# Optimization experiments

Hardware: AMD Instinct MI355X
Metric: run time of the kernel (lower is better)

## Reference

```python
import jax, jax.numpy as jnp
import numpy as np

B, S, D = 8, 4096, 256
L, H = 4, 8
HD = D // H  # head_dim = 32
EPS = 1e-5


def layer_norm(x, gamma, beta):
    mu = jnp.mean(x, axis=-1, keepdims=True)
    var = jnp.mean(jnp.square(x - mu), axis=-1, keepdims=True)
    return (x - mu) * jax.lax.rsqrt(var + EPS) * gamma + beta


def setup_inputs() -> dict:
    key = jax.random.key(0)
    ks = jax.random.split(key, 9)
    sc = 0.02
    x = jax.random.normal(ks[0], (B, S, D), dtype=jnp.float32)
    # per-head projection weights, torch Linear convention: (out=head_dim, in=D)
    Wq = jax.random.normal(ks[1], (L, H, HD, D), dtype=jnp.float32) * sc
    Wk = jax.random.normal(ks[2], (L, H, HD, D), dtype=jnp.float32) * sc
    Wv = jax.random.normal(ks[3], (L, H, HD, D), dtype=jnp.float32) * sc
    W1 = jax.random.normal(ks[4], (L, D, D), dtype=jnp.float32) * sc
    b1 = jax.random.normal(ks[5], (L, D), dtype=jnp.float32) * sc
    W2 = jax.random.normal(ks[6], (L, D, D), dtype=jnp.float32) * sc
    b2 = jax.random.normal(ks[7], (L, D), dtype=jnp.float32) * sc
    gamma = jnp.ones((D,), dtype=jnp.float32)
    beta = jnp.zeros((D,), dtype=jnp.float32)
    return {"processed_grid_repr": x, "Wq": Wq, "Wk": Wk, "Wv": Wv,
            "W1": W1, "b1": b1, "W2": W2, "b2": b2,
            "gamma": gamma, "beta": beta}


def reference(processed_grid_repr, Wq, Wk, Wv, W1, b1, W2, b2, gamma, beta):
    out = processed_grid_repr  # (B, S, D)
    scale = 1.0 / jnp.sqrt(jnp.float32(S))  # original scales by sqrt(seq_len)
    for l in range(L):
        h = layer_norm(out, gamma, beta)
        # all heads at once: (B, H, S, HD)
        Q = jnp.einsum('bsd,hed->bhse', h, Wq[l])
        K = jnp.einsum('bsd,hed->bhse', h, Wk[l])
        V = jnp.einsum('bsd,hed->bhse', h, Wv[l])
        # original does key.reshape(B, HD, S) (a RESHAPE, not a transpose)
        Kr = K.reshape(B, H, HD, S)
        # original einsum 'bqq,bqd->bqd' only uses the diagonal of QK^r,
        # so compute only the diagonal: diag[b,h,q] = sum_e Q[b,h,q,e]*Kr[b,h,e,q]
        diag = jnp.einsum('bhse,bhes->bhs', Q, Kr) * scale
        attn = diag[..., None] * V  # (B, H, S, HD)
        # concat heads along last dim (head order preserved)
        msa_out = attn.transpose(0, 2, 1, 3).reshape(B, S, D)
        attended = msa_out + out
        m = layer_norm(attended, gamma, beta)
        m = jax.nn.gelu(m @ W1[l].T + b1[l], approximate=False)
        m = jax.nn.gelu(m @ W2[l].T + b2[l], approximate=False)
        out = m + attended
    # final: layer norm of CLS-like token 0
    return layer_norm(out[:, 0, :], gamma, beta)  # (B, D)
```

## Files before the change

kernel.cpp:

```cpp
#include <hip/hip_runtime.h>
#include <hip/hip_bf16.h>
#include <hip/hip_fp16.h>

typedef _Float16 half_t;
typedef _Float16 half8 __attribute__((ext_vector_type(8)));
typedef _Float16 half4 __attribute__((ext_vector_type(4)));
typedef float f32x4 __attribute__((ext_vector_type(4)));

#define BB 8
#define SS 4096
#define DD 256
#define HH 8
#define LL 4
#define MTOT (BB*SS)

__device__ inline float gelu_f(float v) { return 0.5f * v * (1.0f + erff(v * 0.70710678118f)); }
__device__ inline half8 splat8(half_t v) { return (half8){v, v, v, v, v, v, v, v}; }

__device__ __forceinline__ void gload16(const half_t* g, half_t* l) {
    __builtin_amdgcn_global_load_lds(
        (const __attribute__((address_space(1))) void*)g,
        (__attribute__((address_space(3))) void*)l, 16, 0, 0);
}

__global__ __launch_bounds__(256) void prep_weights(
    const float* __restrict__ Wq, const float* __restrict__ Wk, const float* __restrict__ Wv,
    const float* __restrict__ W1, const float* __restrict__ b1,
    const float* __restrict__ W2, const float* __restrict__ b2,
    const float* __restrict__ gamma, const float* __restrict__ beta,
    half_t* __restrict__ Wall, half_t* __restrict__ W1h, half_t* __restrict__ W2h,
    float* __restrict__ bqkv, float* __restrict__ b1f, float* __restrict__ b2f)
{
    int blk = blockIdx.x;
    int l = blk / 5, type = blk % 5;
    int o = threadIdx.x;
    const float* src = (type == 0 ? Wq : type == 1 ? Wk : type == 2 ? Wv : type == 3 ? W1 : W2)
                       + ((size_t)l * 256 + o) * 256;
    half_t* dsth = (type < 3) ? Wall + ((size_t)(l * 3 + type) * 256 + o) * 256
                 : (type == 3) ? W1h + ((size_t)l * 256 + o) * 256
                               : W2h + ((size_t)l * 256 + o) * 256;
    float acc = 0.f;
    for (int d4 = 0; d4 < 64; ++d4) {
        float4 w = *(const float4*)(src + d4 * 4);
        half4 hv;
        if (type == 4) {
            hv = half4{ (half_t)w.x, (half_t)w.y, (half_t)w.z, (half_t)w.w };
        } else {
            float4 g = *(const float4*)(gamma + d4 * 4);
            float4 bt = *(const float4*)(beta + d4 * 4);
            acc += w.x * bt.x + w.y * bt.y + w.z * bt.z + w.w * bt.w;
            hv = half4{ (half_t)(w.x * g.x), (half_t)(w.y * g.y), (half_t)(w.z * g.z), (half_t)(w.w * g.w) };
        }
        *(half4*)(dsth + d4 * 4) = hv;
    }
    if (type < 3) bqkv[(l * 3 + type) * 256 + o] = acc;
    else if (type == 3) b1f[l * 256 + o] = b1[l * 256 + o] + acc;
    else b2f[l * 256 + o] = b2[l * 256 + o];
}

__global__ __launch_bounds__(256) void cvt_x(const float* __restrict__ in, half_t* __restrict__ out) {
    int i = (blockIdx.x * 256 + threadIdx.x) * 4;
    float4 v = *(const float4*)(in + i);
    half4 h = { (half_t)v.x, (half_t)v.y, (half_t)v.z, (half_t)v.w };
    *(half4*)(out + i) = h;
}

__global__ __launch_bounds__(256) void row_stats(const half_t* __restrict__ in,
                                                 float2* __restrict__ st) {
    int wave = threadIdx.x >> 6, lane = threadIdx.x & 63;
    int row = blockIdx.x * 4 + wave;
    size_t base = (size_t)row * DD + lane * 4;
    half4 x4 = *(const half4*)(in + base);
    float a0 = x4[0], a1 = x4[1], a2 = x4[2], a3 = x4[3];
    float s1 = a0 + a1 + a2 + a3;
    float s2 = a0 * a0 + a1 * a1 + a2 * a2 + a3 * a3;
    #pragma unroll
    for (int m = 32; m; m >>= 1) {
        s1 += __shfl_xor(s1, m);
        s2 += __shfl_xor(s2, m);
    }
    if (lane == 0) {
        float mu = s1 * (1.0f / DD);
        float var = s2 * (1.0f / DD) - mu * mu;
        st[row] = make_float2(mu, rsqrtf(var + 1e-5f));
    }
}

__device__ inline void xcd_remap(int& bx, int& by, int& bz) {
    int lin = blockIdx.x + gridDim.x * (blockIdx.y + gridDim.y * blockIdx.z);
    int nyz = gridDim.y * gridDim.z;
    int xcd = lin & 7;
    int slot = lin >> 3;
    int yz = slot % nyz;
    int xi = slot / nyz;
    bx = xcd + 8 * xi;
    by = yz % gridDim.y;
    bz = yz / gridDim.y;
}

template<int NORM, int EPI>
__global__ __launch_bounds__(256) void gemm128(const half_t* __restrict__ A,
                                               const float2* __restrict__ statsA,
                                               const half_t* __restrict__ Wbase,
                                               const float* __restrict__ biasBase,
                                               const half_t* __restrict__ resid,
                                               half_t* __restrict__ o0,
                                               half_t* __restrict__ o1,
                                               half_t* __restrict__ o2) {
    const int t = threadIdx.x, lane = t & 63, wavei = t >> 6;
    const int wm = wavei >> 1, wn = wavei & 1, r = lane & 15, g = lane >> 4;
    int bx, by, bz;
    xcd_remap(bx, by, bz);
    const int row0 = bx * 128, col0 = by * 128;
    const half_t* W = Wbase + (size_t)bz * 65536;
    const float* bias = biasBase + bz * 256;
    half_t* outp = (bz == 0) ? o0 : ((bz == 1) ? o1 : o2);

    __shared__ __align__(16) half_t lds[2][16384];

    const half_t* Ag = A + (size_t)row0 * DD;
    const half_t* Wg = W + (size_t)col0 * DD;

    half8 sA[4], bA[4];
    if (NORM) {
        #pragma unroll
        for (int mt = 0; mt < 4; ++mt) {
            float2 st = statsA[row0 + wm * 64 + mt * 16 + r];
            sA[mt] = splat8((half_t)st.y);
            bA[mt] = splat8((half_t)(-st.x * st.y));
        }
    }

    int rowS[4], chS[4];
    #pragma unroll
    for (int i = 0; i < 4; ++i) {
        int G = i * 256 + t;
        rowS[i] = G >> 3;
        chS[i] = ((G & 7) ^ (rowS[i] & 7)) * 8;
    }

    #pragma unroll
    for (int i = 0; i < 4; ++i) {
        int G = i * 256 + t;
        gload16(Ag + (size_t)rowS[i] * DD + chS[i], &lds[0][G * 8]);
        gload16(Wg + (size_t)rowS[i] * DD + chS[i], &lds[0][8192 + G * 8]);
    }
    __syncthreads();

    f32x4 acc[4][4];
    #pragma unroll
    for (int i = 0; i < 4; ++i)
        #pragma unroll
        for (int j = 0; j < 4; ++j) acc[i][j] = (f32x4){0.f, 0.f, 0.f, 0.f};

    #pragma unroll
    for (int stp = 0; stp < 4; ++stp) {
        const int cur = stp & 1;
        if (stp < 3) {
            int kk = (stp + 1) * 64;
            #pragma unroll
            for (int i = 0; i < 4; ++i) {
                int G = i * 256 + t;
                gload16(Ag + (size_t)rowS[i] * DD + kk + chS[i], &lds[cur ^ 1][G * 8]);
                gload16(Wg + (size_t)rowS[i] * DD + kk + chS[i], &lds[cur ^ 1][8192 + G * 8]);
            }
        }
        #pragma unroll
        for (int ks = 0; ks < 2; ++ks) {
            half8 af[4], bf[4];
            #pragma unroll
            for (int mt = 0; mt < 4; ++mt) {
                int rw = wm * 64 + mt * 16 + r;
                int cc = (ks * 4 + g) ^ (rw & 7);
                half8 raw = *(const half8*)&lds[cur][rw * 64 + cc * 8];
                af[mt] = NORM ? (half8)(raw * sA[mt] + bA[mt]) : raw;
            }
            #pragma unroll
            for (int nt = 0; nt < 4; ++nt) {
                int rw = wn * 64 + nt * 16 + r;
                int cc = (ks * 4 + g) ^ (rw & 7);
                bf[nt] = *(const half8*)&lds[cur][8192 + rw * 64 + cc * 8];
            }
            #pragma unroll
            for (int mt = 0; mt < 4; ++mt)
                #pragma unroll
                for (int nt = 0; nt < 4; ++nt)
                    acc[mt][nt] = __builtin_amdgcn_mfma_f32_16x16x32_f16(af[mt], bf[nt], acc[mt][nt], 0, 0, 0);
        }
        __syncthreads();
    }

    half_t* ldsT = &lds[0][0];
    #pragma unroll
    for (int mt = 0; mt < 4; ++mt) {
        #pragma unroll
        for (int nt = 0; nt < 4; ++nt) {
            int colL = wn * 64 + nt * 16 + r;
            float bv = bias[col0 + colL];
            #pragma unroll
            for (int j = 0; j < 4; ++j) {
                int rowL = wm * 64 + mt * 16 + g * 4 + j;
                float v = acc[mt][nt][j] + bv;
                if (EPI != 0) v = gelu_f(v);
                ldsT[rowL * 128 + (colL ^ ((rowL & 12) << 2))] = (half_t)v;
            }
        }
    }
    __syncthreads();
    const int l15 = lane & 15, lg = lane >> 4;
    #pragma unroll
    for (int i = 0; i < 8; ++i) {
        int rowL = wavei * 32 + lg * 8 + i;
        int colL = l15 * 8;
        half8 v = *(const half8*)&ldsT[rowL * 128 + (colL ^ ((rowL & 12) << 2))];
        size_t off = (size_t)(row0 + rowL) * DD + col0 + colL;
        if (EPI == 2) {
            half8 rsd = *(const half8*)&resid[off];
            #pragma unroll
            for (int q = 0; q < 8; ++q) v[q] = (half_t)((float)v[q] + (float)rsd[q]);
        }
        *(half8*)&outp[off] = v;
    }
}

__global__ __launch_bounds__(256) void diag_tiled(const half_t* __restrict__ Q,
                                                  const half_t* __restrict__ K,
                                                  float* __restrict__ dg) {
    int blk = blockIdx.x;
    int sblk = blk & 15, h = (blk >> 4) & 7, b = blk >> 7;
    int t = threadIdx.x;
    __shared__ __align__(16) half_t kt[256 * 32];
    int r0b = sblk * 8;
    {
        int e = t >> 3, del = t & 7;
        const half_t* kp = K + ((size_t)b * SS + e * 128 + r0b + del) * DD + h * 32;
        int4* dst = (int4*)&kt[t * 32];
        const int4* sp = (const int4*)kp;
        dst[0] = sp[0]; dst[1] = sp[1]; dst[2] = sp[2]; dst[3] = sp[3];
    }
    __syncthreads();
    int s = sblk * 256 + t;
    const half8* q8 = (const half8*)(Q + ((size_t)b * SS + s) * DD + h * 32);
    int cs = t & 31, ds = t >> 5;
    float sum = 0.f;
    #pragma unroll
    for (int v = 0; v < 4; ++v) {
        half8 qq = q8[v];
        #pragma unroll
        for (int j = 0; j < 8; ++j) {
            int e = v * 8 + j;
            sum += (float)qq[j] * (float)kt[(e * 8 + ds) * 32 + cs];
        }
    }
    dg[((size_t)b << 15) | ((size_t)h << 12) | s] = sum * 0.015625f;
}

__global__ __launch_bounds__(256) void attn_stat(const half_t* __restrict__ resid,
                                                 const half_t* __restrict__ V,
                                                 const float* __restrict__ dg,
                                                 half_t* __restrict__ att,
                                                 float2* __restrict__ st2) {
    int wave = threadIdx.x >> 6, lane = threadIdx.x & 63;
    int row = blockIdx.x * 4 + wave;
    int b = row >> 12, s = row & (SS - 1);
    int h = lane >> 3;
    float dgv = dg[((size_t)b << 15) | ((size_t)h << 12) | s];
    size_t base = (size_t)row * DD + lane * 4;
    half4 rs4 = *(const half4*)(resid + base);
    half4 v4 = *(const half4*)(V + base);
    float a0 = (float)rs4[0] + dgv * (float)v4[0];
    float a1 = (float)rs4[1] + dgv * (float)v4[1];
    float a2 = (float)rs4[2] + dgv * (float)v4[2];
    float a3 = (float)rs4[3] + dgv * (float)v4[3];
    half4 at = { (half_t)a0, (half_t)a1, (half_t)a2, (half_t)a3 };
    *(half4*)(att + base) = at;
    float s1 = a0 + a1 + a2 + a3;
    float s2 = a0 * a0 + a1 * a1 + a2 * a2 + a3 * a3;
    #pragma unroll
    for (int m = 32; m; m >>= 1) {
        s1 += __shfl_xor(s1, m);
        s2 += __shfl_xor(s2, m);
    }
    if (lane == 0) {
        float mu = s1 * (1.0f / DD);
        float var = s2 * (1.0f / DD) - mu * mu;
        st2[row] = make_float2(mu, rsqrtf(var + 1e-5f));
    }
}

__global__ __launch_bounds__(256) void final_ln_kernel(const half_t* __restrict__ cur,
                                                       float* __restrict__ out,
                                                       const float* __restrict__ gamma,
                                                       const float* __restrict__ beta) {
    int b = blockIdx.x;
    int d = threadIdx.x;
    float x = (float)cur[(size_t)b * SS * DD + d];
    float s1 = x, s2 = x * x;
    #pragma unroll
    for (int m = 32; m; m >>= 1) {
        s1 += __shfl_xor(s1, m);
        s2 += __shfl_xor(s2, m);
    }
    __shared__ float ls1[4], ls2[4];
    int wave = threadIdx.x >> 6, lane = threadIdx.x & 63;
    if (lane == 0) { ls1[wave] = s1; ls2[wave] = s2; }
    __syncthreads();
    float t1 = ls1[0] + ls1[1] + ls1[2] + ls1[3];
    float t2 = ls2[0] + ls2[1] + ls2[2] + ls2[3];
    float mu = t1 * (1.0f / DD);
    float var = t2 * (1.0f / DD) - mu * mu;
    float rs = rsqrtf(var + 1e-5f);
    out[(size_t)b * DD + d] = (x - mu) * rs * gamma[d] + beta[d];
}

extern "C" void kernel_launch(void* const* d_in, const int* in_sizes, int n_in,
                              void* d_out, int out_size, void* d_ws, size_t ws_size,
                              hipStream_t stream) {
    const float* x     = (const float*)d_in[0];
    const float* Wq    = (const float*)d_in[1];
    const float* Wk    = (const float*)d_in[2];
    const float* Wv    = (const float*)d_in[3];
    const float* W1    = (const float*)d_in[4];
    const float* b1    = (const float*)d_in[5];
    const float* W2    = (const float*)d_in[6];
    const float* b2    = (const float*)d_in[7];
    const float* gamma = (const float*)d_in[8];
    const float* beta  = (const float*)d_in[9];

    char* p = (char*)d_ws;
    half_t* x16  = (half_t*)p; p += (size_t)MTOT * DD * 2;
    half_t* cur  = (half_t*)p; p += (size_t)MTOT * DD * 2;
    half_t* att  = (half_t*)p; p += (size_t)MTOT * DD * 2;
    half_t* Qb   = (half_t*)p; p += (size_t)MTOT * DD * 2;
    half_t* Kb   = (half_t*)p; p += (size_t)MTOT * DD * 2;
    half_t* Vb   = (half_t*)p; p += (size_t)MTOT * DD * 2;
    half_t* m1   = (half_t*)p; p += (size_t)MTOT * DD * 2;
    float*  dgp  = (float*)p;  p += (size_t)BB * HH * SS * 4;
    float2* stA  = (float2*)p; p += (size_t)MTOT * 8;
    float2* stB  = (float2*)p; p += (size_t)MTOT * 8;
    half_t* Wall = (half_t*)p; p += (size_t)LL * 3 * 65536 * 2;
    half_t* W1h  = (half_t*)p; p += (size_t)LL * 65536 * 2;
    half_t* W2h  = (half_t*)p; p += (size_t)LL * 65536 * 2;
    float*  bqkv = (float*)p;  p += (size_t)LL * 3 * 256 * 4;
    float*  b1f  = (float*)p;  p += (size_t)LL * 256 * 4;
    float*  b2f  = (float*)p;  p += (size_t)LL * 256 * 4;

    prep_weights<<<LL * 5, 256, 0, stream>>>(Wq, Wk, Wv, W1, b1, W2, b2, gamma, beta,
                                             Wall, W1h, W2h, bqkv, b1f, b2f);
    cvt_x<<<8192, 256, 0, stream>>>(x, x16);

    const half_t* curin = x16;
    for (int l = 0; l < LL; ++l) {
        row_stats<<<MTOT / 4, 256, 0, stream>>>(curin, stA);
        gemm128<1, 0><<<dim3(256, 2, 3), 256, 0, stream>>>(
            curin, stA, Wall + (size_t)l * 3 * 65536, bqkv + l * 3 * 256, nullptr, Qb, Kb, Vb);
        diag_tiled<<<1024, 256, 0, stream>>>(Qb, Kb, dgp);
        attn_stat<<<MTOT / 4, 256, 0, stream>>>(curin, Vb, dgp, att, stB);
        gemm128<1, 1><<<dim3(256, 2, 1), 256, 0, stream>>>(
            att, stB, W1h + (size_t)l * 65536, b1f + l * 256, nullptr, m1, m1, m1);
        gemm128<0, 2><<<dim3(256, 2, 1), 256, 0, stream>>>(
            m1, nullptr, W2h + (size_t)l * 65536, b2f + l * 256, att, cur, cur, cur);
        curin = cur;
    }
    final_ln_kernel<<<BB, 256, 0, stream>>>(cur, (float*)d_out, gamma, beta);
}
```

Before: 369.7 us.

## Fuse FFN GEMMs into one kernel keeping intermediate in LDS, fold row stats

Replaces the two separate FFN GEMM launches with one kernel. Each block takes 64 rows, applies the layer-norm affine on the fly, computes GELU(W1) into shared memory, then runs the W2 GEMM, residual add and GELU from shared memory. It writes the new activations and their row statistics for the next layer's LN, which removes the separate row_stats launch. The input conversion is also merged with the first row-stats pass. This avoids the m1 round trip through global memory and several launches, at the cost of about 80KB of LDS per block (lower occupancy) and a 64-row tile with 512 blocks.

After: 362.3 us. -2.0%, faster.

```diff
diff --git a/kernel.cpp b/kernel.cpp
--- a/kernel.cpp
+++ b/kernel.cpp
@@ -58,22 +58,17 @@
     else b2f[l * 256 + o] = b2[l * 256 + o];
 }
 
-__global__ __launch_bounds__(256) void cvt_x(const float* __restrict__ in, half_t* __restrict__ out) {
-    int i = (blockIdx.x * 256 + threadIdx.x) * 4;
-    float4 v = *(const float4*)(in + i);
-    half4 h = { (half_t)v.x, (half_t)v.y, (half_t)v.z, (half_t)v.w };
-    *(half4*)(out + i) = h;
-}
-
-__global__ __launch_bounds__(256) void row_stats(const half_t* __restrict__ in,
-                                                 float2* __restrict__ st) {
+__global__ __launch_bounds__(256) void cvt_x_stats(const float* __restrict__ in,
+                                                   half_t* __restrict__ out,
+                                                   float2* __restrict__ st) {
     int wave = threadIdx.x >> 6, lane = threadIdx.x & 63;
     int row = blockIdx.x * 4 + wave;
-    size_t base = (size_t)row * DD + lane * 4;
-    half4 x4 = *(const half4*)(in + base);
-    float a0 = x4[0], a1 = x4[1], a2 = x4[2], a3 = x4[3];
-    float s1 = a0 + a1 + a2 + a3;
-    float s2 = a0 * a0 + a1 * a1 + a2 * a2 + a3 * a3;
+    const float* ip = in + (size_t)row * DD + lane * 4;
+    float4 v = *(const float4*)ip;
+    half4 h = { (half_t)v.x, (half_t)v.y, (half_t)v.z, (half_t)v.w };
+    *(half4*)(out + (size_t)row * DD + lane * 4) = h;
+    float s1 = v.x + v.y + v.z + v.w;
+    float s2 = v.x * v.x + v.y * v.y + v.z * v.z + v.w * v.w;
     #pragma unroll
     for (int m = 32; m; m >>= 1) {
         s1 += __shfl_xor(s1, m);
@@ -288,6 +283,207 @@
     }
 }
 
+__global__ __launch_bounds__(256) void ffn_fused(const half_t* __restrict__ att_g,
+                                                 const float2* __restrict__ stB,
+                                                 const half_t* __restrict__ W1l,
+                                                 const float* __restrict__ b1l,
+                                                 const half_t* __restrict__ W2l,
+                                                 const float* __restrict__ b2l,
+                                                 half_t* __restrict__ cur,
+                                                 float2* __restrict__ stA) {
+    const int t = threadIdx.x, lane = t & 63, wavei = t >> 6;
+    const int wm = wavei >> 1, wn = wavei & 1, r = lane & 15, g = lane >> 4;
+    int bx, by, bz;
+    xcd_remap(bx, by, bz);
+    const int row0 = bx * 64;
+
+    __shared__ __align__(16) half_t Araw[64 * 256];
+    __shared__ __align__(16) half_t M1[64 * 256];
+    __shared__ __align__(16) half_t Wb[2][64 * 64];
+
+    #pragma unroll
+    for (int i = 0; i < 8; ++i) {
+        int G = i * 256 + t;
+        int row = G >> 5, c = G & 31;
+        int cs = (c & 24) | ((c & 7) ^ (row & 7));
+        gload16(att_g + (size_t)(row0 + row) * DD + cs * 8, &Araw[G * 8]);
+    }
+    #pragma unroll
+    for (int i = 0; i < 2; ++i) {
+        int G = i * 256 + t;
+        int wrow = G >> 3, wc = (G & 7) ^ (wrow & 7);
+        gload16(W1l + (size_t)wrow * DD + wc * 8, &Wb[0][G * 8]);
+    }
+    __syncthreads();
+
+    half8 sA[2], bA[2];
+    #pragma unroll
+    for (int mt = 0; mt < 2; ++mt) {
+        float2 st = stB[row0 + wm * 32 + mt * 16 + r];
+        sA[mt] = splat8((half_t)st.y);
+        bA[mt] = splat8((half_t)(-st.x * st.y));
+    }
+
+    f32x4 acc[2][2];
+    #pragma unroll
+    for (int i = 0; i < 2; ++i)
+        #pragma unroll
+        for (int j = 0; j < 2; ++j) acc[i][j] = (f32x4){0.f, 0.f, 0.f, 0.f};
+
+    #pragma unroll
+    for (int sub = 0; sub < 16; ++sub) {
+        const int ncol = sub >> 2, stp = sub & 3, cb = sub & 1;
+        if (sub < 15) {
+            const int nc2 = (sub + 1) >> 2, st2 = (sub + 1) & 3;
+            #pragma unroll
+            for (int i = 0; i < 2; ++i) {
+                int G = i * 256 + t;
+                int wrow = G >> 3, wc = (G & 7) ^ (wrow & 7);
+                gload16(W1l + (size_t)(nc2 * 64 + wrow) * DD + st2 * 64 + wc * 8, &Wb[cb ^ 1][G * 8]);
+            }
+        }
+        #pragma unroll
+        for (int ks = 0; ks < 2; ++ks) {
+            half8 af[2], bf[2];
+            #pragma unroll
+            for (int mt = 0; mt < 2; ++mt) {
+                int rw = wm * 32 + mt * 16 + r;
+                int kc = stp * 8 + ks * 4 + g;
+                int p = (kc & 24) | ((kc & 7) ^ (rw & 7));
+                half8 raw = *(const half8*)&Araw[rw * 256 + p * 8];
+                af[mt] = raw * sA[mt] + bA[mt];
+            }
+            #pragma unroll
+            for (int nt = 0; nt < 2; ++nt) {
+                int wr = wn * 32 + nt * 16 + r;
+                int cc = (ks * 4 + g) ^ (wr & 7);
+                bf[nt] = *(const half8*)&Wb[cb][wr * 64 + cc * 8];
+            }
+            #pragma unroll
+            for (int mt = 0; mt < 2; ++mt)
+                #pragma unroll
+                for (int nt = 0; nt < 2; ++nt)
+                    acc[mt][nt] = __builtin_amdgcn_mfma_f32_16x16x32_f16(af[mt], bf[nt], acc[mt][nt], 0, 0, 0);
+        }
+        if (stp == 3) {
+            #pragma unroll
+            for (int mt = 0; mt < 2; ++mt) {
+                #pragma unroll
+                for (int nt = 0; nt < 2; ++nt) {
+                    int colL = ncol * 64 + wn * 32 + nt * 16 + r;
+                    float bv = b1l[colL];
+                    #pragma unroll
+                    for (int j = 0; j < 4; ++j) {
+                        int rowL = wm * 32 + mt * 16 + g * 4 + j;
+                        float v = gelu_f(acc[mt][nt][j] + bv);
+                        int c = colL >> 3;
+                        int p = (c & 24) | ((c & 7) ^ (rowL & 7));
+                        M1[rowL * 256 + p * 8 + (colL & 7)] = (half_t)v;
+                    }
+                    acc[mt][nt] = (f32x4){0.f, 0.f, 0.f, 0.f};
+                }
+            }
+        }
+        __syncthreads();
+    }
+
+    #pragma unroll
+    for (int i = 0; i < 2; ++i) {
+        int G = i * 256 + t;
+        int wrow = G >> 3, wc = (G & 7) ^ (wrow & 7);
+        gload16(W2l + (size_t)wrow * DD + wc * 8, &Wb[0][G * 8]);
+    }
+    __syncthreads();
+
+    f32x4 a2[4][2][2];
+    #pragma unroll
+    for (int n = 0; n < 4; ++n)
+        #pragma unroll
+        for (int i = 0; i < 2; ++i)
+            #pragma unroll
+            for (int j = 0; j < 2; ++j) a2[n][i][j] = (f32x4){0.f, 0.f, 0.f, 0.f};
+
+    #pragma unroll
+    for (int sub = 0; sub < 16; ++sub) {
+        const int stp = sub >> 2, nc = sub & 3, cb = sub & 1;
+        if (sub < 15) {
+            const int stq = (sub + 1) >> 2, ncq = (sub + 1) & 3;
+            #pragma unroll
+            for (int i = 0; i < 2; ++i) {
+                int G = i * 256 + t;
+                int wrow = G >> 3, wc = (G & 7) ^ (wrow & 7);
+                gload16(W2l + (size_t)(ncq * 64 + wrow) * DD + stq * 64 + wc * 8, &Wb[cb ^ 1][G * 8]);
+            }
+        }
+        #pragma unroll
+        for (int ks = 0; ks < 2; ++ks) {
+            half8 af[2], bf[2];
+            #pragma unroll
+            for (int mt = 0; mt < 2; ++mt) {
+                int rw = wm * 32 + mt * 16 + r;
+                int kc = stp * 8 + ks * 4 + g;
+                int p = (kc & 24) | ((kc & 7) ^ (rw & 7));
+                af[mt] = *(const half8*)&M1[rw * 256 + p * 8];
+            }
+            #pragma unroll
+            for (int nt = 0; nt < 2; ++nt) {
+                int wr = wn * 32 + nt * 16 + r;
+                int cc = (ks * 4 + g) ^ (wr & 7);
+                bf[nt] = *(const half8*)&Wb[cb][wr * 64 + cc * 8];
+            }
+            #pragma unroll
+            for (int mt = 0; mt < 2; ++mt)
+                #pragma unroll
+                for (int nt = 0; nt < 2; ++nt)
+                    a2[nc][mt][nt] = __builtin_amdgcn_mfma_f32_16x16x32_f16(af[mt], bf[nt], a2[nc][mt][nt], 0, 0, 0);
+        }
+        __syncthreads();
+    }
+
+    #pragma unroll
+    for (int nc = 0; nc < 4; ++nc) {
+        #pragma unroll
+        for (int mt = 0; mt < 2; ++mt) {
+            #pragma unroll
+            for (int nt = 0; nt < 2; ++nt) {
+                int colL = nc * 64 + wn * 32 + nt * 16 + r;
+                float bv = b2l[colL];
+                int ca = colL >> 3;
+                #pragma unroll
+                for (int j = 0; j < 4; ++j) {
+                    int rowL = wm * 32 + mt * 16 + g * 4 + j;
+                    int pa = (ca & 24) | ((ca & 7) ^ (rowL & 7));
+                    float rv = (float)Araw[rowL * 256 + pa * 8 + (colL & 7)];
+                    float v = gelu_f(a2[nc][mt][nt][j] + bv) + rv;
+                    M1[rowL * 256 + pa * 8 + (colL & 7)] = (half_t)v;
+                }
+            }
+        }
+    }
+    __syncthreads();
+    #pragma unroll
+    for (int i = 0; i < 8; ++i) {
+        int G = i * 256 + t;
+        int rowL = G >> 5, c = G & 31;
+        int p = (c & 24) | ((c & 7) ^ (rowL & 7));
+        half8 v = *(const half8*)&M1[rowL * 256 + p * 8];
+        *(half8*)&cur[(size_t)(row0 + rowL) * DD + c * 8] = v;
+        float s1 = 0.f, s2 = 0.f;
+        #pragma unroll
+        for (int q = 0; q < 8; ++q) { float f = (float)v[q]; s1 += f; s2 += f * f; }
+        #pragma unroll
+        for (int m = 1; m <= 16; m <<= 1) {
+            s1 += __shfl_xor(s1, m);
+            s2 += __shfl_xor(s2, m);
+        }
+        if ((t & 31) == 0) {
+            float mu = s1 * (1.0f / DD);
+            float var = s2 * (1.0f / DD) - mu * mu;
+            stA[row0 + rowL] = make_float2(mu, rsqrtf(var + 1e-5f));
+        }
+    }
+}
+
 __global__ __launch_bounds__(256) void final_ln_kernel(const half_t* __restrict__ cur,
                                                        float* __restrict__ out,
                                                        const float* __restrict__ gamma,
@@ -334,7 +530,6 @@
     half_t* Qb   = (half_t*)p; p += (size_t)MTOT * DD * 2;
     half_t* Kb   = (half_t*)p; p += (size_t)MTOT * DD * 2;
     half_t* Vb   = (half_t*)p; p += (size_t)MTOT * DD * 2;
-    half_t* m1   = (half_t*)p; p += (size_t)MTOT * DD * 2;
     float*  dgp  = (float*)p;  p += (size_t)BB * HH * SS * 4;
     float2* stA  = (float2*)p; p += (size_t)MTOT * 8;
     float2* stB  = (float2*)p; p += (size_t)MTOT * 8;
@@ -347,19 +542,16 @@
 
     prep_weights<<<LL * 5, 256, 0, stream>>>(Wq, Wk, Wv, W1, b1, W2, b2, gamma, beta,
                                              Wall, W1h, W2h, bqkv, b1f, b2f);
-    cvt_x<<<8192, 256, 0, stream>>>(x, x16);
+    cvt_x_stats<<<MTOT / 4, 256, 0, stream>>>(x, x16, stA);
 
     const half_t* curin = x16;
     for (int l = 0; l < LL; ++l) {
-        row_stats<<<MTOT / 4, 256, 0, stream>>>(curin, stA);
         gemm128<1, 0><<<dim3(256, 2, 3), 256, 0, stream>>>(
             curin, stA, Wall + (size_t)l * 3 * 65536, bqkv + l * 3 * 256, nullptr, Qb, Kb, Vb);
         diag_tiled<<<1024, 256, 0, stream>>>(Qb, Kb, dgp);
         attn_stat<<<MTOT / 4, 256, 0, stream>>>(curin, Vb, dgp, att, stB);
-        gemm128<1, 1><<<dim3(256, 2, 1), 256, 0, stream>>>(
-            att, stB, W1h + (size_t)l * 65536, b1f + l * 256, nullptr, m1, m1, m1);
-        gemm128<0, 2><<<dim3(256, 2, 1), 256, 0, stream>>>(
-            m1, nullptr, W2h + (size_t)l * 65536, b2f + l * 256, att, cur, cur, cur);
+        ffn_fused<<<512, 256, 0, stream>>>(att, stB, W1h + (size_t)l * 65536, b1f + l * 256,
+                                           W2h + (size_t)l * 65536, b2f + l * 256, cur, stA);
         curin = cur;
     }
     final_ln_kernel<<<BB, 256, 0, stream>>>(cur, (float*)d_out, gamma, beta);
```

## Fuse LayerNorm row statistics into producer kernels and drop row_stats pass

Applied to the files above, without the earlier changes.

The separate row_stats kernel is removed. Partial sums (sum and sum of squares) are now computed in the epilogue of the W2 GEMM, with one buffer per column-half block, and in the input conversion kernel. The consuming GEMM combines the two partials and derives mean and rstd itself. This saves one full read of the activation tensor plus a kernel launch per layer, at the cost of extra shuffles in the GEMM epilogue and a less stable variance formula.

Measured after the change: 362.1 us. 2.1% less time.

```diff
diff --git a/kernel.cpp b/kernel.cpp
--- a/kernel.cpp
+++ b/kernel.cpp
@@ -58,31 +58,26 @@
     else b2f[l * 256 + o] = b2[l * 256 + o];
 }
 
-__global__ __launch_bounds__(256) void cvt_x(const float* __restrict__ in, half_t* __restrict__ out) {
-    int i = (blockIdx.x * 256 + threadIdx.x) * 4;
-    float4 v = *(const float4*)(in + i);
-    half4 h = { (half_t)v.x, (half_t)v.y, (half_t)v.z, (half_t)v.w };
-    *(half4*)(out + i) = h;
-}
-
-__global__ __launch_bounds__(256) void row_stats(const half_t* __restrict__ in,
-                                                 float2* __restrict__ st) {
+__global__ __launch_bounds__(256) void cvt_x_stats(const float* __restrict__ in,
+                                                   half_t* __restrict__ out,
+                                                   float2* __restrict__ st0,
+                                                   float2* __restrict__ st1) {
     int wave = threadIdx.x >> 6, lane = threadIdx.x & 63;
     int row = blockIdx.x * 4 + wave;
-    size_t base = (size_t)row * DD + lane * 4;
-    half4 x4 = *(const half4*)(in + base);
-    float a0 = x4[0], a1 = x4[1], a2 = x4[2], a3 = x4[3];
-    float s1 = a0 + a1 + a2 + a3;
-    float s2 = a0 * a0 + a1 * a1 + a2 * a2 + a3 * a3;
+    const float* ip = in + (size_t)row * DD + lane * 4;
+    float4 v = *(const float4*)ip;
+    half4 h = { (half_t)v.x, (half_t)v.y, (half_t)v.z, (half_t)v.w };
+    *(half4*)(out + (size_t)row * DD + lane * 4) = h;
+    float s1 = v.x + v.y + v.z + v.w;
+    float s2 = v.x * v.x + v.y * v.y + v.z * v.z + v.w * v.w;
     #pragma unroll
     for (int m = 32; m; m >>= 1) {
         s1 += __shfl_xor(s1, m);
         s2 += __shfl_xor(s2, m);
     }
     if (lane == 0) {
-        float mu = s1 * (1.0f / DD);
-        float var = s2 * (1.0f / DD) - mu * mu;
-        st[row] = make_float2(mu, rsqrtf(var + 1e-5f));
+        st0[row] = make_float2(s1, s2);
+        st1[row] = make_float2(0.f, 0.f);
     }
 }
 
@@ -98,15 +93,18 @@
     bz = yz / gridDim.y;
 }
 
-template<int NORM, int EPI>
+template<int NORM, int EPI, int STATS>
 __global__ __launch_bounds__(256) void gemm128(const half_t* __restrict__ A,
-                                               const float2* __restrict__ statsA,
+                                               const float2* __restrict__ st0,
+                                               const float2* __restrict__ st1,
                                                const half_t* __restrict__ Wbase,
                                                const float* __restrict__ biasBase,
                                                const half_t* __restrict__ resid,
                                                half_t* __restrict__ o0,
                                                half_t* __restrict__ o1,
-                                               half_t* __restrict__ o2) {
+                                               half_t* __restrict__ o2,
+                                               float2* __restrict__ outSt0,
+                                               float2* __restrict__ outSt1) {
     const int t = threadIdx.x, lane = t & 63, wavei = t >> 6;
     const int wm = wavei >> 1, wn = wavei & 1, r = lane & 15, g = lane >> 4;
     int bx, by, bz;
@@ -125,9 +123,14 @@
     if (NORM) {
         #pragma unroll
         for (int mt = 0; mt < 4; ++mt) {
-            float2 st = statsA[row0 + wm * 64 + mt * 16 + r];
-            sA[mt] = splat8((half_t)st.y);
-            bA[mt] = splat8((half_t)(-st.x * st.y));
+            int row = row0 + wm * 64 + mt * 16 + r;
+            float2 p0 = st0[row], p1 = st1[row];
+            float s1 = p0.x + p1.x, s2 = p0.y + p1.y;
+            float mu = s1 * (1.0f / DD);
+            float var = s2 * (1.0f / DD) - mu * mu;
+            float rs = rsqrtf(var + 1e-5f);
+            sA[mt] = splat8((half_t)rs);
+            bA[mt] = splat8((half_t)(-mu * rs));
         }
     }
 
@@ -208,6 +211,7 @@
     }
     __syncthreads();
     const int l15 = lane & 15, lg = lane >> 4;
+    float2* outSt = (by == 0) ? outSt0 : outSt1;
     #pragma unroll
     for (int i = 0; i < 8; ++i) {
         int rowL = wavei * 32 + lg * 8 + i;
@@ -220,6 +224,17 @@
             for (int q = 0; q < 8; ++q) v[q] = (half_t)((float)v[q] + (float)rsd[q]);
         }
         *(half8*)&outp[off] = v;
+        if (STATS) {
+            float s1 = 0.f, s2 = 0.f;
+            #pragma unroll
+            for (int q = 0; q < 8; ++q) { float f = (float)v[q]; s1 += f; s2 += f * f; }
+            #pragma unroll
+            for (int m = 1; m <= 8; m <<= 1) {
+                s1 += __shfl_xor(s1, m);
+                s2 += __shfl_xor(s2, m);
+            }
+            if (l15 == 0) outSt[row0 + rowL] = make_float2(s1, s2);
+        }
     }
 }
 
@@ -259,7 +274,8 @@
                                                  const half_t* __restrict__ V,
                                                  const float* __restrict__ dg,
                                                  half_t* __restrict__ att,
-                                                 float2* __restrict__ st2) {
+                                                 float2* __restrict__ st0,
+                                                 float2* __restrict__ st1) {
     int wave = threadIdx.x >> 6, lane = threadIdx.x & 63;
     int row = blockIdx.x * 4 + wave;
     int b = row >> 12, s = row & (SS - 1);
@@ -282,9 +298,8 @@
         s2 += __shfl_xor(s2, m);
     }
     if (lane == 0) {
-        float mu = s1 * (1.0f / DD);
-        float var = s2 * (1.0f / DD) - mu * mu;
-        st2[row] = make_float2(mu, rsqrtf(var + 1e-5f));
+        st0[row] = make_float2(s1, s2);
+        st1[row] = make_float2(0.f, 0.f);
     }
 }
 
@@ -336,8 +351,10 @@
     half_t* Vb   = (half_t*)p; p += (size_t)MTOT * DD * 2;
     half_t* m1   = (half_t*)p; p += (size_t)MTOT * DD * 2;
     float*  dgp  = (float*)p;  p += (size_t)BB * HH * SS * 4;
-    float2* stA  = (float2*)p; p += (size_t)MTOT * 8;
-    float2* stB  = (float2*)p; p += (size_t)MTOT * 8;
+    float2* stA0 = (float2*)p; p += (size_t)MTOT * 8;
+    float2* stA1 = (float2*)p; p += (size_t)MTOT * 8;
+    float2* stB0 = (float2*)p; p += (size_t)MTOT * 8;
+    float2* stB1 = (float2*)p; p += (size_t)MTOT * 8;
     half_t* Wall = (half_t*)p; p += (size_t)LL * 3 * 65536 * 2;
     half_t* W1h  = (half_t*)p; p += (size_t)LL * 65536 * 2;
     half_t* W2h  = (half_t*)p; p += (size_t)LL * 65536 * 2;
@@ -347,19 +364,21 @@
 
     prep_weights<<<LL * 5, 256, 0, stream>>>(Wq, Wk, Wv, W1, b1, W2, b2, gamma, beta,
                                              Wall, W1h, W2h, bqkv, b1f, b2f);
-    cvt_x<<<8192, 256, 0, stream>>>(x, x16);
+    cvt_x_stats<<<MTOT / 4, 256, 0, stream>>>(x, x16, stA0, stA1);
 
     const half_t* curin = x16;
     for (int l = 0; l < LL; ++l) {
-        row_stats<<<MTOT / 4, 256, 0, stream>>>(curin, stA);
-        gemm128<1, 0><<<dim3(256, 2, 3), 256, 0, stream>>>(
-            curin, stA, Wall + (size_t)l * 3 * 65536, bqkv + l * 3 * 256, nullptr, Qb, Kb, Vb);
+        gemm128<1, 0, 0><<<dim3(256, 2, 3), 256, 0, stream>>>(
+            curin, stA0, stA1, Wall + (size_t)l * 3 * 65536, bqkv + l * 3 * 256,
+            nullptr, Qb, Kb, Vb, nullptr, nullptr);
         diag_tiled<<<1024, 256, 0, stream>>>(Qb, Kb, dgp);
-        attn_stat<<<MTOT / 4, 256, 0, stream>>>(curin, Vb, dgp, att, stB);
-        gemm128<1, 1><<<dim3(256, 2, 1), 256, 0, stream>>>(
-            att, stB, W1h + (size_t)l * 65536, b1f + l * 256, nullptr, m1, m1, m1);
-        gemm128<0, 2><<<dim3(256, 2, 1), 256, 0, stream>>>(
-            m1, nullptr, W2h + (size_t)l * 65536, b2f + l * 256, att, cur, cur, cur);
+        attn_stat<<<MTOT / 4, 256, 0, stream>>>(curin, Vb, dgp, att, stB0, stB1);
+        gemm128<1, 1, 0><<<dim3(256, 2, 1), 256, 0, stream>>>(
+            att, stB0, stB1, W1h + (size_t)l * 65536, b1f + l * 256,
+            nullptr, m1, m1, m1, nullptr, nullptr);
+        gemm128<0, 2, 1><<<dim3(256, 2, 1), 256, 0, stream>>>(
+            m1, nullptr, nullptr, W2h + (size_t)l * 65536, b2f + l * 256,
+            att, cur, cur, cur, stA0, stA1);
         curin = cur;
     }
     final_ln_kernel<<<BB, 256, 0, stream>>>(cur, (float*)d_out, gamma, beta);
```
